# Optimization experiments

Measured on AMD Instinct MI355X. Metric: run time of the kernel, lower is better.

The kernel has to match this reference:

```python
import jax, jax.numpy as jnp
import numpy as np

B, FG, ANT, D = 256, 4, 32, 1024   # batch, freq_groups, antennas, d_model
H, DK = 16, 64                      # n_heads, d_k; inner_dim = H*DK = 1024
INNER = H * DK


def setup_inputs() -> dict:
    key = jax.random.key(0)
    ks = jax.random.split(key, 17)
    s = 0.02
    inp = {"x": jax.random.normal(ks[0], (B, FG * ANT, D), dtype=jnp.float32)}
    names = ["ant_q", "ant_k", "ant_v", "ant_out", "freq_q", "freq_k", "freq_v", "freq_out"]
    for i, n in enumerate(names):
        # all layers are D->INNER or INNER->D; here D == INNER == 1024
        inp[n + "_w"] = jax.random.normal(ks[1 + 2 * i], (D, INNER), dtype=jnp.float32) * s
        inp[n + "_b"] = jnp.zeros((INNER,), dtype=jnp.float32)
    return inp


def _elu1(x):
    return jax.nn.elu(x) + 1.0


def _linear_attention(x, wq, bq, wk, bk, wv, bv):
    # x: (Baug, Lax, D)
    Baug, Lax, _ = x.shape
    Q = _elu1((x @ wq + bq).reshape(Baug, Lax, H, DK))
    K = _elu1((x @ wk + bk).reshape(Baug, Lax, H, DK))
    V = (x @ wv + bv).reshape(Baug, Lax, H, DK)
    KV = jnp.einsum('blhd,blhe->bhde', K, V)      # (Baug, H, DK, DK)
    out = jnp.einsum('blhd,bhde->blhe', Q, KV)    # (Baug, Lax, H, DK)
    return out.reshape(Baug, Lax, INNER)


def reference(x, ant_q_w, ant_q_b, ant_k_w, ant_k_b, ant_v_w, ant_v_b,
              ant_out_w, ant_out_b, freq_q_w, freq_q_b, freq_k_w, freq_k_b,
              freq_v_w, freq_v_b, freq_out_w, freq_out_b):
    # L == ANT*FG, no CLS token; dropout is identity (eval mode)
    grid_ant = x.reshape(B * FG, ANT, D)
    ant = _linear_attention(grid_ant, ant_q_w, ant_q_b, ant_k_w, ant_k_b, ant_v_w, ant_v_b)
    grid_ant = grid_ant + (ant @ ant_out_w + ant_out_b)
    # (B, FG, ANT, D) -> (B, ANT, FG, D)
    grid = grid_ant.reshape(B, FG, ANT, D).transpose(0, 2, 1, 3)
    grid_freq = grid.reshape(B * ANT, FG, D)
    frq = _linear_attention(grid_freq, freq_q_w, freq_q_b, freq_k_w, freq_k_b, freq_v_w, freq_v_b)
    grid_freq = grid_freq + (frq @ freq_out_w + freq_out_b)
    # back to (B, FG, ANT, D) -> (B, L, D)
    out = grid_freq.reshape(B, ANT, FG, D).transpose(0, 2, 1, 3).reshape(B, FG * ANT, D)
    return out
```

## Files before the change

### kernel.cpp

```cpp
#include <hip/hip_runtime.h>
#include <math.h>


#define MTOT 32768
#define DM 1024

using half8   = __attribute__((ext_vector_type(8))) _Float16;
using h2      = __attribute__((ext_vector_type(2))) _Float16;
using floatx4 = __attribute__((ext_vector_type(4))) float;

#define ACT_NONE 0
#define ACT_ELU1 1
#define REMAP_NONE 0
#define REMAP_A2F 1
#define REMAP_F2O 2

__device__ __forceinline__ void gload16(const void* g, void* lds) {
  __builtin_amdgcn_global_load_lds(
      (const __attribute__((address_space(1))) unsigned int*)g,
      (__attribute__((address_space(3))) unsigned int*)lds, 16, 0, 0);
}

__device__ __forceinline__ float fdot2f(h2 a, h2 b, float c) {
#if __has_builtin(__builtin_amdgcn_fdot2)
  return __builtin_amdgcn_fdot2(a, b, c, false);
#else
  return fmaf((float)a[0], (float)b[0], fmaf((float)a[1], (float)b[1], c));
#endif
}

template<int ACT, int REMAP, bool RES, bool OF32, bool OF16>
__global__ __launch_bounds__(256) void gemm_k(
    const _Float16* __restrict__ A, const _Float16* __restrict__ W,
    const float* __restrict__ bias, const _Float16* __restrict__ resid,
    float rs, float* __restrict__ Cf, _Float16* __restrict__ Ch,
    float sin_s, float sout_s)
{
  __shared__ _Float16 As[8192];
  __shared__ _Float16 Bs[8192];

  const int t = threadIdx.x, w = t >> 6, l = t & 63;
  const int bx = blockIdx.x;
  const int m0 = (((bx & 7) << 5) + (bx >> 3)) * 128;
  const int n0 = blockIdx.y * 128;
  const int lr = l & 15, ls = l >> 4;
  const int wrow = (w >> 1) * 64, wcol = (w & 1) * 64;

  const int lrow = l >> 3;
  const int lsl  = ((l & 7) ^ (lrow & 7)) * 8;

  int aoff[2][4], boff[2][4];
#pragma unroll
  for (int kk = 0; kk < 2; ++kk)
#pragma unroll
    for (int m = 0; m < 4; ++m) {
      int ra = wrow + m * 16 + lr;
      aoff[kk][m] = ra * 128 + (((kk * 4 + ls) ^ (ra & 7)) << 4);
      int rb = wcol + m * 16 + lr;
      boff[kk][m] = rb * 128 + (((kk * 4 + ls) ^ (rb & 7)) << 4);
    }

  floatx4 acc[4][4];
#pragma unroll
  for (int m = 0; m < 4; ++m)
#pragma unroll
    for (int n = 0; n < 4; ++n) acc[m][n] = (floatx4)0.f;

  const char* AsC = (const char*)As;
  const char* BsC = (const char*)Bs;

  for (int k0 = 0; k0 < DM; k0 += 64) {
    if (k0) __syncthreads();
#pragma unroll
    for (int i = 0; i < 4; ++i) {
      int u = w * 4 + i;
      int row = u * 8 + lrow;
      gload16(A + (size_t)(m0 + row) * DM + k0 + lsl, (char*)As + u * 1024);
      gload16(W + (size_t)(n0 + row) * DM + k0 + lsl, (char*)Bs + u * 1024);
    }
    __syncthreads();

#pragma unroll
    for (int kk = 0; kk < 2; ++kk) {
      half8 af[4], bf[4];
#pragma unroll
      for (int m = 0; m < 4; ++m) af[m] = *(const half8*)(AsC + aoff[kk][m]);
#pragma unroll
      for (int n = 0; n < 4; ++n) bf[n] = *(const half8*)(BsC + boff[kk][n]);
#pragma unroll
      for (int m = 0; m < 4; ++m)
#pragma unroll
        for (int n = 0; n < 4; ++n)
          acc[m][n] = __builtin_amdgcn_mfma_f32_16x16x32_f16(af[m], bf[n], acc[m][n], 0, 0, 0);
    }
  }

  float bb[4];
#pragma unroll
  for (int n = 0; n < 4; ++n) bb[n] = bias[n0 + wcol + n * 16 + lr];

#pragma unroll
  for (int m = 0; m < 4; ++m)
#pragma unroll
    for (int n = 0; n < 4; ++n)
#pragma unroll
      for (int j = 0; j < 4; ++j) {
        int rt = wrow + m * 16 + ls * 4 + j;
        int ct = wcol + n * 16 + lr;
        float v = acc[m][n][j] * sin_s + bb[n];
        if (RES) v += rs * (float)resid[(size_t)(m0 + rt) * DM + n0 + ct];
        if (ACT == ACT_ELU1) v = (v > 0.f) ? (v + 1.f) : expf(v);
        acc[m][n][j] = v;
      }
  if (RES && REMAP != REMAP_NONE) __syncthreads();

#pragma unroll
  for (int m = 0; m < 4; ++m)
#pragma unroll
    for (int n = 0; n < 4; ++n)
#pragma unroll
      for (int j = 0; j < 4; ++j) {
        int rt = wrow + m * 16 + ls * 4 + j;
        int ct = wcol + n * 16 + lr;
        int mg = m0 + rt, ng = n0 + ct;
        int srw;
        if (REMAP == REMAP_NONE) {
          srw = mg;
        } else if (REMAP == REMAP_A2F) {
          int b = mg >> 7, fg = (mg >> 5) & 3, ant = mg & 31;
          srw = b * 128 + ant * 4 + fg;
        } else {
          int b = mg >> 7, ant = (mg >> 2) & 31, fg = mg & 3;
          srw = b * 128 + fg * 32 + ant;
        }
        float v = acc[m][n][j];
        if (OF32) Cf[(size_t)srw * DM + ng] = v;
        if (OF16) Ch[(size_t)srw * DM + ng] = (_Float16)(v * sout_s);
      }
}

__global__ __launch_bounds__(256) void linattn32_k(
    _Float16* __restrict__ Q, const _Float16* __restrict__ K,
    const _Float16* __restrict__ V, float sout)
{
  __shared__ _Float16 Qs[32][64];
  __shared__ _Float16 Ks[32][64];
  __shared__ _Float16 Vs[32][64];
  __shared__ float Ss[32][33];

  const int g = blockIdx.x, h = blockIdx.y;
  const size_t base = (size_t)g * 32 * DM + h * 64;
  const int t = threadIdx.x;

  {
    const int row = t >> 3, ch = (t & 7) * 8;
    half8 q8 = *(const half8*)(Q + base + (size_t)row * DM + ch);
    half8 k8 = *(const half8*)(K + base + (size_t)row * DM + ch);
    half8 v8 = *(const half8*)(V + base + (size_t)row * DM + ch);
    *(half8*)&Qs[row][ch ^ ((row & 7) * 8)] = q8;
    *(half8*)&Ks[row][ch ^ (((row >> 2) & 7) * 8)] = k8;
    *(half8*)&Vs[row][ch] = v8;
  }
  __syncthreads();

  {
    const int tt = t >> 3, sg = t & 7;
    const int xq = (tt & 7) * 8, xk = sg * 8;
    float acc[4] = {};
#pragma unroll
    for (int jj = 0; jj < 32; ++jj) {
      h2 qq = *(const h2*)&Qs[tt][(2 * jj) ^ xq];
#pragma unroll
      for (int si = 0; si < 4; ++si) {
        h2 kk = *(const h2*)&Ks[sg * 4 + si][(2 * jj) ^ xk];
        acc[si] = fdot2f(qq, kk, acc[si]);
      }
    }
#pragma unroll
    for (int si = 0; si < 4; ++si) Ss[tt][sg * 4 + si] = acc[si];
  }
  __syncthreads();

  {
    const int tt = t >> 3, e0 = (t & 7) * 8;
    float o[8] = {};
#pragma unroll
    for (int s = 0; s < 32; ++s) {
      float sv = Ss[tt][s];
      half8 vv = *(const half8*)&Vs[s][e0];
#pragma unroll
      for (int e = 0; e < 8; ++e) o[e] = fmaf(sv, (float)vv[e], o[e]);
    }
    half8 r;
#pragma unroll
    for (int e = 0; e < 8; ++e) r[e] = (_Float16)(o[e] * sout);
    *(half8*)(Q + base + (size_t)tt * DM + e0) = r;
  }
}

__global__ __launch_bounds__(256) void linattn4_k(
    _Float16* __restrict__ Q, const _Float16* __restrict__ K,
    const _Float16* __restrict__ V, float sout)
{
  __shared__ _Float16 Qs[4][1024];
  __shared__ _Float16 Ks[4][1024];
  __shared__ _Float16 Vs[4][1024];
  __shared__ float Ss[16][4][5];

  const int g = blockIdx.x;
  const size_t base = (size_t)g * 4 * DM;
  const int t = threadIdx.x;

  {
    const int off = t * 16;
    const int row = off >> 10, col = off & 1023;
    const int h = col >> 6, d = col & 63, x = (h & 7) * 8;
    const int c0 = h * 64 + (d ^ x), c1 = h * 64 + ((d + 8) ^ x);
    half8 q0 = *(const half8*)(Q + base + off);
    half8 q1 = *(const half8*)(Q + base + off + 8);
    half8 k0 = *(const half8*)(K + base + off);
    half8 k1 = *(const half8*)(K + base + off + 8);
    half8 v0 = *(const half8*)(V + base + off);
    half8 v1 = *(const half8*)(V + base + off + 8);
    *(half8*)&Qs[row][c0] = q0; *(half8*)&Qs[row][c1] = q1;
    *(half8*)&Ks[row][c0] = k0; *(half8*)&Ks[row][c1] = k1;
    *(half8*)&Vs[row][c0] = v0; *(half8*)&Vs[row][c1] = v1;
  }
  __syncthreads();

  {
    const int h = t >> 4, tt = (t >> 2) & 3, s = t & 3;
    const int x = (h & 7) * 8;
    const _Float16* qp = &Qs[tt][h * 64];
    const _Float16* kp = &Ks[s][h * 64];
    float acc = 0.f;
#pragma unroll
    for (int jj = 0; jj < 32; ++jj) {
      int dd = (2 * jj) ^ x;
      acc = fdot2f(*(const h2*)(qp + dd), *(const h2*)(kp + dd), acc);
    }
    Ss[h][tt][s] = acc;
  }
  __syncthreads();

  {
    const int tt = t >> 6, cg = t & 63;
    const int h = cg >> 2, e0 = (cg & 3) * 16, x = (h & 7) * 8;
    const float* sp = Ss[h][tt];
    float o[16] = {};
#pragma unroll
    for (int s = 0; s < 4; ++s) {
      float sv = sp[s];
      half8 va = *(const half8*)&Vs[s][h * 64 + (e0 ^ x)];
      half8 vb = *(const half8*)&Vs[s][h * 64 + ((e0 + 8) ^ x)];
#pragma unroll
      for (int e = 0; e < 8; ++e) {
        o[e]     = fmaf(sv, (float)va[e], o[e]);
        o[e + 8] = fmaf(sv, (float)vb[e], o[e + 8]);
      }
    }
    half8 r0, r1;
#pragma unroll
    for (int e = 0; e < 8; ++e) {
      r0[e] = (_Float16)(o[e] * sout);
      r1[e] = (_Float16)(o[e + 8] * sout);
    }
    _Float16* dst = Q + base + (size_t)tt * DM + h * 64 + e0;
    *(half8*)dst = r0;
    *(half8*)(dst + 8) = r1;
  }
}

struct WPtrs { const float* p[8]; };

__global__ __launch_bounds__(256) void transpose_w8_k(
    WPtrs ws, _Float16* __restrict__ wt)
{
  __shared__ float tile[32][33];
  const float* W = ws.p[blockIdx.z];
  _Float16* Wt = wt + (size_t)DM * DM * blockIdx.z;
  const int tx = threadIdx.x & 31, ty = threadIdx.x >> 5;
  const int k0 = blockIdx.x * 32, n0 = blockIdx.y * 32;
#pragma unroll
  for (int r = 0; r < 4; ++r)
    tile[ty + r * 8][tx] = W[(size_t)(k0 + ty + r * 8) * DM + n0 + tx];
  __syncthreads();
#pragma unroll
  for (int r = 0; r < 4; ++r)
    Wt[(size_t)(n0 + ty + r * 8) * DM + k0 + tx] = (_Float16)tile[tx][ty + r * 8];
}

__global__ __launch_bounds__(256) void convf2h_k(
    const float* __restrict__ x, _Float16* __restrict__ xh, int n8)
{
  for (int i = blockIdx.x * blockDim.x + threadIdx.x; i < n8;
       i += gridDim.x * blockDim.x) {
    float4 a = ((const float4*)x)[i * 2];
    float4 b = ((const float4*)x)[i * 2 + 1];
    half8 h;
    h[0] = (_Float16)a.x; h[1] = (_Float16)a.y; h[2] = (_Float16)a.z; h[3] = (_Float16)a.w;
    h[4] = (_Float16)b.x; h[5] = (_Float16)b.y; h[6] = (_Float16)b.z; h[7] = (_Float16)b.w;
    ((half8*)xh)[i] = h;
  }
}

extern "C" void kernel_launch(void* const* d_in, const int* in_sizes, int n_in,
                              void* d_out, int out_size, void* d_ws, size_t ws_size,
                              hipStream_t stream)
{
  const float* x   = (const float*)d_in[0];
  WPtrs wp;
  for (int j = 0; j < 8; ++j) wp.p[j] = (const float*)d_in[1 + 2 * j];
  const float* aqb = (const float*)d_in[2];  const float* akb = (const float*)d_in[4];
  const float* avb = (const float*)d_in[6];  const float* aob = (const float*)d_in[8];
  const float* fqb = (const float*)d_in[10]; const float* fkb = (const float*)d_in[12];
  const float* fvb = (const float*)d_in[14]; const float* fob = (const float*)d_in[16];
  float* out = (float*)d_out;

  const size_t NE = (size_t)MTOT * DM;
  _Float16* xh = (_Float16*)d_ws;
  _Float16* Qh = xh + NE;
  _Float16* Kh = Qh + NE;
  _Float16* Vh = Kh + NE;
  _Float16* wt = Vh + NE;
  const size_t WSZ = (size_t)DM * DM;

  dim3 gg(MTOT / 128, DM / 128), gb(256);

  convf2h_k<<<2048, gb, 0, stream>>>(x, xh, (int)(NE / 8));
  transpose_w8_k<<<dim3(32, 32, 8), gb, 0, stream>>>(wp, wt);

  const float S = 0.0625f;

  gemm_k<ACT_ELU1, REMAP_NONE, false, false, true><<<gg, gb, 0, stream>>>(
      xh, wt + WSZ * 0, aqb, nullptr, 0.f, nullptr, Qh, 1.f, 1.f);
  gemm_k<ACT_ELU1, REMAP_NONE, false, false, true><<<gg, gb, 0, stream>>>(
      xh, wt + WSZ * 1, akb, nullptr, 0.f, nullptr, Kh, 1.f, 1.f);
  gemm_k<ACT_NONE, REMAP_NONE, false, false, true><<<gg, gb, 0, stream>>>(
      xh, wt + WSZ * 2, avb, nullptr, 0.f, nullptr, Vh, 1.f, 1.f);
  linattn32_k<<<dim3(1024, 16), gb, 0, stream>>>(Qh, Kh, Vh, S);
  gemm_k<ACT_NONE, REMAP_A2F, true, false, true><<<gg, gb, 0, stream>>>(
      Qh, wt + WSZ * 3, aob, xh, 1.f, nullptr, xh, 16.f, S);

  gemm_k<ACT_ELU1, REMAP_NONE, false, false, true><<<gg, gb, 0, stream>>>(
      xh, wt + WSZ * 4, fqb, nullptr, 0.f, nullptr, Qh, 16.f, S);
  gemm_k<ACT_ELU1, REMAP_NONE, false, false, true><<<gg, gb, 0, stream>>>(
      xh, wt + WSZ * 5, fkb, nullptr, 0.f, nullptr, Kh, 16.f, S);
  gemm_k<ACT_NONE, REMAP_NONE, false, false, true><<<gg, gb, 0, stream>>>(
      xh, wt + WSZ * 6, fvb, nullptr, 0.f, nullptr, Vh, 16.f, S);
  linattn4_k<<<8192, gb, 0, stream>>>(Qh, Kh, Vh, S);
  gemm_k<ACT_NONE, REMAP_F2O, true, true, false><<<gg, gb, 0, stream>>>(
      Qh, wt + WSZ * 7, fob, xh, 16.f, out, nullptr, 65536.f, 1.f);
}
```

Measured before the change: 969.8 us.

## Triple-buffer GEMM LDS pipeline with 256x128 tiles and 8 waves

Replaces the single-buffered GEMM main loop, which loaded and then synchronized every K step, with a three-stage software pipeline. Global-to-LDS loads for future K tiles are issued ahead and throttled with vmcnt waits and raw barriers. The block tile grows to 256x128 with 512 threads, so each B tile is reused by more rows, and MFMA sections are wrapped in raised wave priority. This uses about 144KB of LDS per block, which limits the kernel to one block per CU, and it changes the grid mapping for all eight GEMM launches.

```diff
diff --git a/kernel.cpp b/kernel.cpp
--- a/kernel.cpp
+++ b/kernel.cpp
@@ -15,10 +15,14 @@
 #define REMAP_A2F 1
 #define REMAP_F2O 2
 
-__device__ __forceinline__ void gload16(const void* g, void* lds) {
+#define VMWAIT(n) asm volatile("s_waitcnt vmcnt(" #n ")" ::: "memory")
+#define SBAR() do { __builtin_amdgcn_s_barrier(); \
+                    __builtin_amdgcn_sched_barrier(0); } while (0)
+
+__device__ __forceinline__ void gload16(const void* g, void* ldsp) {
   __builtin_amdgcn_global_load_lds(
       (const __attribute__((address_space(1))) unsigned int*)g,
-      (__attribute__((address_space(3))) unsigned int*)lds, 16, 0, 0);
+      (__attribute__((address_space(3))) unsigned int*)ldsp, 16, 0, 0);
 }
 
 __device__ __forceinline__ float fdot2f(h2 a, h2 b, float c) {
@@ -30,24 +34,24 @@
 }
 
 template<int ACT, int REMAP, bool RES, bool OF32, bool OF16>
-__global__ __launch_bounds__(256) void gemm_k(
+__global__ __launch_bounds__(512, 2) void gemm_k(
     const _Float16* __restrict__ A, const _Float16* __restrict__ W,
     const float* __restrict__ bias, const _Float16* __restrict__ resid,
     float rs, float* __restrict__ Cf, _Float16* __restrict__ Ch,
     float sin_s, float sout_s)
 {
-  __shared__ _Float16 As[8192];
-  __shared__ _Float16 Bs[8192];
+  __shared__ __align__(16) char lds[147456];
 
   const int t = threadIdx.x, w = t >> 6, l = t & 63;
   const int bx = blockIdx.x;
-  const int m0 = (((bx & 7) << 5) + (bx >> 3)) * 128;
+  const int m0 = (((bx & 7) << 4) + (bx >> 3)) * 256;
   const int n0 = blockIdx.y * 128;
   const int lr = l & 15, ls = l >> 4;
   const int wrow = (w >> 1) * 64, wcol = (w & 1) * 64;
 
-  const int lrow = l >> 3;
-  const int lsl  = ((l & 7) ^ (lrow & 7)) * 8;
+  const int trow = t >> 3;
+  const int tsk  = ((t & 7) ^ (trow & 7)) * 8;
+  char* const ldsw = lds + w * 1024;
 
   int aoff[2][4], boff[2][4];
 #pragma unroll
@@ -66,34 +70,50 @@
 #pragma unroll
     for (int n = 0; n < 4; ++n) acc[m][n] = (floatx4)0.f;
 
-  const char* AsC = (const char*)As;
-  const char* BsC = (const char*)Bs;
-
-  for (int k0 = 0; k0 < DM; k0 += 64) {
-    if (k0) __syncthreads();
-#pragma unroll
-    for (int i = 0; i < 4; ++i) {
-      int u = w * 4 + i;
-      int row = u * 8 + lrow;
-      gload16(A + (size_t)(m0 + row) * DM + k0 + lsl, (char*)As + u * 1024);
-      gload16(W + (size_t)(n0 + row) * DM + k0 + lsl, (char*)Bs + u * 1024);
-    }
-    __syncthreads();
-
+  auto stage = [&](int kt, int p) {
+    const int kb = kt * 64;
+#pragma unroll
+    for (int i = 0; i < 4; ++i)
+      gload16(A + (size_t)(m0 + i * 64 + trow) * DM + kb + tsk,
+              ldsw + p * 32768 + i * 8192);
+#pragma unroll
+    for (int i = 0; i < 2; ++i)
+      gload16(W + (size_t)(n0 + i * 64 + trow) * DM + kb + tsk,
+              ldsw + 98304 + p * 16384 + i * 8192);
+  };
+
+  auto compute = [&](int p) {
+    const char* Ab = lds + p * 32768;
+    const char* Bb = lds + 98304 + p * 16384;
 #pragma unroll
     for (int kk = 0; kk < 2; ++kk) {
       half8 af[4], bf[4];
 #pragma unroll
-      for (int m = 0; m < 4; ++m) af[m] = *(const half8*)(AsC + aoff[kk][m]);
-#pragma unroll
-      for (int n = 0; n < 4; ++n) bf[n] = *(const half8*)(BsC + boff[kk][n]);
+      for (int m = 0; m < 4; ++m) af[m] = *(const half8*)(Ab + aoff[kk][m]);
+#pragma unroll
+      for (int n = 0; n < 4; ++n) bf[n] = *(const half8*)(Bb + boff[kk][n]);
+      __builtin_amdgcn_s_setprio(1);
 #pragma unroll
       for (int m = 0; m < 4; ++m)
 #pragma unroll
         for (int n = 0; n < 4; ++n)
-          acc[m][n] = __builtin_amdgcn_mfma_f32_16x16x32_f16(af[m], bf[n], acc[m][n], 0, 0, 0);
-    }
-  }
+          acc[m][n] =
+              __builtin_amdgcn_mfma_f32_16x16x32_f16(af[m], bf[n], acc[m][n], 0, 0, 0);
+      __builtin_amdgcn_s_setprio(0);
+    }
+  };
+
+  stage(0, 0);
+  stage(1, 1);
+  for (int t2 = 0; t2 < 14; ++t2) {
+    stage(t2 + 2, (t2 + 2) % 3);
+    VMWAIT(12);
+    SBAR();
+    compute(t2 % 3);
+    SBAR();
+  }
+  VMWAIT(6);  SBAR(); compute(2); SBAR();
+  VMWAIT(0);  SBAR(); compute(0);
 
   float bb[4];
 #pragma unroll
@@ -325,10 +345,10 @@
   _Float16* wt = Vh + NE;
   const size_t WSZ = (size_t)DM * DM;
 
-  dim3 gg(MTOT / 128, DM / 128), gb(256);
-
-  convf2h_k<<<2048, gb, 0, stream>>>(x, xh, (int)(NE / 8));
-  transpose_w8_k<<<dim3(32, 32, 8), gb, 0, stream>>>(wp, wt);
+  dim3 gg(MTOT / 256, DM / 128), gb(512), sb(256);
+
+  convf2h_k<<<2048, sb, 0, stream>>>(x, xh, (int)(NE / 8));
+  transpose_w8_k<<<dim3(32, 32, 8), sb, 0, stream>>>(wp, wt);
 
   const float S = 0.0625f;
 
@@ -338,7 +358,7 @@
       xh, wt + WSZ * 1, akb, nullptr, 0.f, nullptr, Kh, 1.f, 1.f);
   gemm_k<ACT_NONE, REMAP_NONE, false, false, true><<<gg, gb, 0, stream>>>(
       xh, wt + WSZ * 2, avb, nullptr, 0.f, nullptr, Vh, 1.f, 1.f);
-  linattn32_k<<<dim3(1024, 16), gb, 0, stream>>>(Qh, Kh, Vh, S);
+  linattn32_k<<<dim3(1024, 16), sb, 0, stream>>>(Qh, Kh, Vh, S);
   gemm_k<ACT_NONE, REMAP_A2F, true, false, true><<<gg, gb, 0, stream>>>(
       Qh, wt + WSZ * 3, aob, xh, 1.f, nullptr, xh, 16.f, S);
 
@@ -348,7 +368,7 @@
       xh, wt + WSZ * 5, fkb, nullptr, 0.f, nullptr, Kh, 16.f, S);
   gemm_k<ACT_NONE, REMAP_NONE, false, false, true><<<gg, gb, 0, stream>>>(
       xh, wt + WSZ * 6, fvb, nullptr, 0.f, nullptr, Vh, 16.f, S);
-  linattn4_k<<<8192, gb, 0, stream>>>(Qh, Kh, Vh, S);
+  linattn4_k<<<8192, sb, 0, stream>>>(Qh, Kh, Vh, S);
   gemm_k<ACT_NONE, REMAP_F2O, true, true, false><<<gg, gb, 0, stream>>>(
       Qh, wt + WSZ * 7, fob, xh, 16.f, out, nullptr, 65536.f, 1.f);
 }
```

Result: no change. 988.3 us (+1.9%).
